# Optimization experiments

Measured on AMD Instinct MI355X. Metric: run time of the kernel, lower is better.

## Reference

```python
import jax, jax.numpy as jnp
import numpy as np

B, N, K = 4096, 64, 4


def _jump_sum(Ls, rho):
    # sum_k L_k @ rho @ L_k^dagger  (real dtype -> dagger == transpose)
    return jnp.einsum('kij,bjl,kml->bim', Ls, rho, Ls)


def _sandwich(U, rho):
    # U @ rho @ U^dagger
    return jnp.einsum('ij,bjl,ml->bim', U, rho, U)


def setup_inputs() -> dict:
    key = jax.random.key(0)
    k = jax.random.split(key, 6)
    eye = jnp.eye(N, dtype=jnp.float32)
    rho0 = jax.random.normal(k[0], (B, N, N), dtype=jnp.float32)
    # propagators: near-identity perturbations, Um well-conditioned for the LU solve
    U1 = eye + 0.1 * jax.random.normal(k[1], (N, N), dtype=jnp.float32)
    Um = eye + 0.1 * jax.random.normal(k[2], (N, N), dtype=jnp.float32)
    Ls0 = jax.random.normal(k[3], (K, N, N), dtype=jnp.float32)
    Lsmid = jax.random.normal(k[4], (K, N, N), dtype=jnp.float32)
    Ls1 = jax.random.normal(k[5], (K, N, N), dtype=jnp.float32)
    dt = jnp.asarray(0.01, dtype=jnp.float32)
    return {'rho0': rho0, 'U1': U1, 'Um': Um, 'Ls0': Ls0,
            'Lsmid': Lsmid, 'Ls1': Ls1, 'dt': dt}


def reference(rho0, U1, Um, Ls0, Lsmid, Ls1, dt):
    # propagator from t+dt/2 to t+dt via LU solve: solve(Um^T, U1^T)^T
    Um1 = jnp.linalg.solve(Um.T, U1.T).T

    # stage 1
    rho1 = rho0
    # stage 2 (SecondStage, no_jump_0 = Um, Ls = Ls0, aii = 0.5)
    rho2 = _sandwich(Um, rho0 + 0.5 * dt * _jump_sum(Ls0, rho1))
    # stage 3 (SameTimeStage, no_jump_0 = Um, Ls = Lsmid, aii = 0.5)
    rho3 = _sandwich(Um, rho0) + 0.5 * dt * _jump_sum(Lsmid, rho2)
    rho23 = rho2 + rho3
    # stage 4 (RKStage, no_jump_0 = U1, no_jump_i = Um1, Ls = Lsmid, aii = 1.0)
    rho4 = _sandwich(U1, rho0) + _sandwich(Um1, dt * _jump_sum(Lsmid, rho3))

    out = (_sandwich(U1, rho0 + (dt / 6) * _jump_sum(Ls0, rho1))
           + _sandwich(Um1, (dt / 3) * _jump_sum(Lsmid, rho23))
           + (dt / 6) * _jump_sum(Ls1, rho4))
    return out
```

## Files before the change

### kernel.cpp

```cpp
#include <hip/hip_runtime.h>


typedef __attribute__((ext_vector_type(16))) float f32x16;
typedef __attribute__((ext_vector_type(8))) __bf16 bf16x8;

#define MATB 8192

__device__ __forceinline__ unsigned short bf16rne(float x) {
  unsigned u = __builtin_bit_cast(unsigned, x);
  return (unsigned short)((u + 0x7FFFu + ((u >> 16) & 1u)) >> 16);
}
__device__ __forceinline__ float bflo(unsigned u) {
  return __builtin_bit_cast(float, u << 16);
}
__device__ __forceinline__ float bfhi(unsigned u) {
  return __builtin_bit_cast(float, u & 0xFFFF0000u);
}

__device__ __forceinline__ void mm4_gl(f32x16& acc, const char* __restrict__ gP,
                                       const char* ldsQ, int vq, int lh) {
#pragma unroll
  for (int s = 0; s < 4; ++s) {
    bf16x8 a = *(const bf16x8*)(gP + s * 1024);
    bf16x8 b = *(const bf16x8*)(ldsQ + (((2 * s + lh) ^ vq) << 4));
    acc = __builtin_amdgcn_mfma_f32_32x32x16_bf16(a, b, acc, 0, 0, 0);
  }
}
__device__ __forceinline__ void mm4_lg(f32x16& acc, const char* ldsP, int vp,
                                       int lh, const char* __restrict__ gQ) {
#pragma unroll
  for (int s = 0; s < 4; ++s) {
    bf16x8 a = *(const bf16x8*)(ldsP + (((2 * s + lh) ^ vp) << 4));
    bf16x8 b = *(const bf16x8*)(gQ + s * 1024);
    acc = __builtin_amdgcn_mfma_f32_32x32x16_bf16(a, b, acc, 0, 0, 0);
  }
}

__device__ __forceinline__ void wtile(char* base, int ti, int slotc, int coff,
                                      int lh, const f32x16& v) {
#pragma unroll
  for (int r = 0; r < 16; ++r) {
    int row = ti * 32 + 4 * lh + (r & 3) + 8 * (r >> 2);
    int ps = (slotc ^ ((4 * ti + (r >> 2)) & 7)) << 4;
    *(unsigned short*)(base + row * 128 + ps + coff) = bf16rne(v[r]);
  }
}
__device__ __forceinline__ void wtile_rmw(char* base, int ti, int slotc, int coff,
                                          int lh, const f32x16& v, float s) {
#pragma unroll
  for (int r = 0; r < 16; ++r) {
    int row = ti * 32 + 4 * lh + (r & 3) + 8 * (r >> 2);
    int ps = (slotc ^ ((4 * ti + (r >> 2)) & 7)) << 4;
    unsigned short* p = (unsigned short*)(base + row * 128 + ps + coff);
    float old = bflo((unsigned)*p);
    *p = bf16rne(old + s * v[r]);
  }
}

__device__ __forceinline__ void axpy(char* D, const char* A, float s,
                                     const char* B, int tid) {
#pragma unroll
  for (int j = 0; j < 8; ++j) {
    int off = (tid + 256 * j) * 4;
    unsigned a = *(const unsigned*)(A + off);
    unsigned b = *(const unsigned*)(B + off);
    float lo = bflo(a) + s * bflo(b);
    float hi = bfhi(a) + s * bfhi(b);
    *(unsigned*)(D + off) = (unsigned)bf16rne(lo) | ((unsigned)bf16rne(hi) << 16);
  }
}

__global__ __launch_bounds__(256) void kraus_invert(
    const float* __restrict__ U1, const float* __restrict__ Um,
    float* __restrict__ Um1) {
  __shared__ float M[64][66];
  __shared__ float X[64][66];
  int tid = threadIdx.x;
#pragma unroll
  for (int it = 0; it < 16; ++it) {
    int idx = tid + 256 * it;
    int r = idx >> 6, c = idx & 63;
    M[r][c] = Um[idx];
    X[r][c] = (r == c) ? 1.0f : 0.0f;
  }
  __syncthreads();
  for (int k = 0; k < 64; ++k) {
    if (tid < 64) {
      float ip = 1.0f / M[k][k];
      M[k][tid] *= ip;
      X[k][tid] *= ip;
    }
    __syncthreads();
    int r = tid & 63, q = tid >> 6;
    float f = M[r][k];
    __syncthreads();
    if (r != k) {
#pragma unroll
      for (int cc = 0; cc < 16; ++cc) {
        int c = q * 16 + cc;
        M[r][c] -= f * M[k][c];
        X[r][c] -= f * X[k][c];
      }
    }
    __syncthreads();
  }
  for (int it = 0; it < 16; ++it) {
    int idx = tid + 256 * it;
    int i = idx >> 6, j = idx & 63;
    float s = 0.0f;
#pragma unroll 4
    for (int k = 0; k < 64; ++k) s += U1[i * 64 + k] * X[k][j];
    Um1[idx] = s;
  }
}

__global__ __launch_bounds__(256) void kraus_prepack(
    const float* __restrict__ U1, const float* __restrict__ Um,
    const float* __restrict__ Ls0, const float* __restrict__ Lsmid,
    const float* __restrict__ Ls1, float* __restrict__ ws) {
  const float* Um1 = ws;
  unsigned short* dst = (unsigned short*)((char*)ws + 16384);
  int o = blockIdx.x;
  const float* s;
  if (o == 0) s = U1;
  else if (o == 1) s = Um;
  else if (o == 2) s = Um1;
  else if (o < 7) s = Ls0 + (o - 3) * 4096;
  else if (o < 11) s = Lsmid + (o - 7) * 4096;
  else s = Ls1 + (o - 11) * 4096;
  unsigned short* d = dst + o * 4096;
  int tid = threadIdx.x;
#pragma unroll
  for (int j = 0; j < 16; ++j) {
    int idx = tid + 256 * j;
    int f = idx >> 9, l = (idx >> 3) & 63, i = idx & 7;
    int t = f >> 2, ss = f & 3;
    int R = t * 32 + (l & 31);
    int C = ss * 16 + (l >> 5) * 8 + i;
    d[idx] = bf16rne(s[R * 64 + C]);
  }
}

__global__ __launch_bounds__(256, 4) void kraus_main(
    const float* __restrict__ rho0g, const float* __restrict__ dtp,
    const char* __restrict__ gfrag, float* __restrict__ outg) {
  __shared__ __align__(16) char lds[5 * MATB];
  char* B0 = lds;
  char* B1 = B0 + MATB;
  char* B3 = B1 + MATB;
  char* B4 = B3 + MATB;
  char* TMP = B4 + MATB;

  const int tid = threadIdx.x;
  const int l = tid & 63, w = tid >> 6;
  const int ti = w >> 1, tj = w & 1;
  const int l31 = l & 31, lh = l >> 5;
  const int vA = (4 * ti + (l31 >> 3)) & 7;
  const int vB = (4 * tj + (l31 >> 3)) & 7;
  const int rA = (ti * 32 + l31) * 128;
  const int rB = (tj * 32 + l31) * 128;
  const int slotc = 4 * tj + (l31 >> 3), coff = (l31 & 7) * 2;
  const float dt = dtp[0];
  const size_t b = blockIdx.x;
  const char* gA0 = gfrag + ti * 4096 + l * 16;
  const char* gB0 = gfrag + tj * 4096 + l * 16;
#define GA(o) (gA0 + (o) * 8192)
#define GB(o) (gB0 + (o) * 8192)

  {
    const float* src = rho0g + b * 4096 + tid * 16;
    float vals[16];
#pragma unroll
    for (int q = 0; q < 4; ++q) {
      float4 f = *(const float4*)(src + q * 4);
      vals[q * 4 + 0] = f.x; vals[q * 4 + 1] = f.y;
      vals[q * 4 + 2] = f.z; vals[q * 4 + 3] = f.w;
    }
    int r = tid >> 2, c0 = (tid & 3) * 16;
    int sr = r >> 3, cr = (r & 7) * 2;
#pragma unroll
    for (int u = 0; u < 16; ++u) {
      int row = c0 + u;
      int ps = (sr ^ ((row >> 3) & 7)) << 4;
      *(unsigned short*)(B0 + row * 128 + ps + cr) = bf16rne(vals[u]);
    }
  }
  __syncthreads();

  f32x16 outacc = {};

  {
    f32x16 J = {};
    for (int k = 0; k < 4; ++k) {
      if (k) __syncthreads();
      f32x16 t = {};
      mm4_gl(t, GA(3 + k), B0 + rB, vB, lh);
      wtile(TMP, ti, slotc, coff, lh, t);
      __syncthreads();
      mm4_gl(J, GA(3 + k), TMP + rB, vB, lh);
    }
    __syncthreads();
    wtile(B1, ti, slotc, coff, lh, J);
  }
  __syncthreads();

  { f32x16 t = {}; mm4_gl(t, GA(0), B1 + rB, vB, lh); wtile(TMP, ti, slotc, coff, lh, t); }
  __syncthreads();
  { f32x16 s = {}; mm4_lg(s, TMP + rA, vA, lh, GB(0)); outacc += (dt / 6.f) * s; }
  __syncthreads();

  { f32x16 t = {}; mm4_gl(t, GA(0), B0 + rB, vB, lh); wtile(TMP, ti, slotc, coff, lh, t); }
  __syncthreads();
  { f32x16 s = {}; mm4_lg(s, TMP + rA, vA, lh, GB(0)); outacc += s; }
  { f32x16 s = {}; mm4_gl(s, GA(0), TMP + rB, vB, lh); wtile(B4, ti, slotc, coff, lh, s); }

  axpy(B1, B0, 0.5f * dt, B1, tid);
  __syncthreads();

  { f32x16 t = {}; mm4_gl(t, GA(1), B1 + rB, vB, lh); wtile(TMP, ti, slotc, coff, lh, t); }
  __syncthreads();
  { f32x16 s = {}; mm4_gl(s, GA(1), TMP + rB, vB, lh); wtile(B1, ti, slotc, coff, lh, s); }
  __syncthreads();

  { f32x16 t = {}; mm4_gl(t, GA(1), B0 + rB, vB, lh); wtile(TMP, ti, slotc, coff, lh, t); }
  __syncthreads();
  { f32x16 s = {}; mm4_gl(s, GA(1), TMP + rB, vB, lh); wtile(B3, ti, slotc, coff, lh, s); }
  __syncthreads();

  {
    f32x16 J = {};
    for (int k = 0; k < 4; ++k) {
      if (k) __syncthreads();
      f32x16 t = {};
      mm4_gl(t, GA(7 + k), B1 + rB, vB, lh);
      wtile(TMP, ti, slotc, coff, lh, t);
      __syncthreads();
      mm4_gl(J, GA(7 + k), TMP + rB, vB, lh);
    }
    __syncthreads();
    wtile(B0, ti, slotc, coff, lh, J);
  }
  __syncthreads();
  axpy(B1, B3, 0.5f * dt, B0, tid);
  __syncthreads();

  {
    f32x16 J = {};
    for (int k = 0; k < 4; ++k) {
      if (k) __syncthreads();
      f32x16 t = {};
      mm4_gl(t, GA(7 + k), B1 + rB, vB, lh);
      wtile(TMP, ti, slotc, coff, lh, t);
      __syncthreads();
      mm4_gl(J, GA(7 + k), TMP + rB, vB, lh);
    }
    __syncthreads();
    wtile(B3, ti, slotc, coff, lh, J);
  }
  __syncthreads();
  axpy(B1, B0, 1.0f, B3, tid);
  __syncthreads();

  { f32x16 t = {}; mm4_gl(t, GA(2), B1 + rB, vB, lh); wtile(TMP, ti, slotc, coff, lh, t); }
  __syncthreads();
  { f32x16 s = {}; mm4_lg(s, TMP + rA, vA, lh, GB(2)); outacc += (dt / 3.f) * s; }
  __syncthreads();

  { f32x16 t = {}; mm4_gl(t, GA(2), B3 + rB, vB, lh); wtile(TMP, ti, slotc, coff, lh, t); }
  __syncthreads();
  { f32x16 s = {}; mm4_gl(s, GA(2), TMP + rB, vB, lh); wtile_rmw(B4, ti, slotc, coff, lh, s, dt); }
  __syncthreads();

  {
    f32x16 J = {};
    for (int k = 0; k < 4; ++k) {
      if (k) __syncthreads();
      f32x16 t = {};
      mm4_gl(t, GA(11 + k), B4 + rB, vB, lh);
      wtile(TMP, ti, slotc, coff, lh, t);
      __syncthreads();
      mm4_lg(J, TMP + rA, vA, lh, GB(11 + k));
    }
    outacc += (dt / 6.f) * J;
  }

  {
    float* op = outg + b * 4096 + (size_t)(ti * 32 + lh * 4) * 64 + tj * 32 + l31;
#pragma unroll
    for (int r = 0; r < 16; ++r) {
      int row = (r & 3) + 8 * (r >> 2);
      op[row * 64] = outacc[r];
    }
  }
#undef GA
#undef GB
}

extern "C" void kernel_launch(void* const* d_in, const int* in_sizes, int n_in,
                              void* d_out, int out_size, void* d_ws, size_t ws_size,
                              hipStream_t stream) {
  const float* rho0 = (const float*)d_in[0];
  const float* U1 = (const float*)d_in[1];
  const float* Um = (const float*)d_in[2];
  const float* Ls0 = (const float*)d_in[3];
  const float* Lsmid = (const float*)d_in[4];
  const float* Ls1 = (const float*)d_in[5];
  const float* dtp = (const float*)d_in[6];
  float* out = (float*)d_out;
  float* ws = (float*)d_ws;

  const int B = in_sizes[0] >> 12;

  kraus_invert<<<1, 256, 0, stream>>>(U1, Um, ws);
  kraus_prepack<<<15, 256, 0, stream>>>(U1, Um, Ls0, Lsmid, Ls1, ws);
  kraus_main<<<B, 256, 0, stream>>>(rho0, dtp, (const char*)d_ws + 16384, out);
}
```

Before: 232.6 us.

## Double-buffer jump-sum intermediates and merge independent stages to cut barriers

```diff
diff --git a/kernel.cpp b/kernel.cpp
--- a/kernel.cpp
+++ b/kernel.cpp
@@ -164,8 +164,14 @@
   const size_t b = blockIdx.x;
   const char* gA0 = gfrag + ti * 4096 + l * 16;
   const char* gB0 = gfrag + tj * 4096 + l * 16;
-#define GA(o) (gA0 + (o) * 8192)
-#define GB(o) (gB0 + (o) * 8192)
+
+  auto GL = [&](f32x16& acc, int op, const char* q) {
+    mm4_gl(acc, gA0 + op * 8192, q + rB, vB, lh);
+  };
+  auto LG = [&](f32x16& acc, const char* p, int op) {
+    mm4_lg(acc, p + rA, vA, lh, gB0 + op * 8192);
+  };
+  auto WT = [&](char* dst, const f32x16& v) { wtile(dst, ti, slotc, coff, lh, v); };
 
   {
     const float* src = rho0g + b * 4096 + tid * 16;
@@ -191,97 +197,68 @@
 
   {
     f32x16 J = {};
-    for (int k = 0; k < 4; ++k) {
-      if (k) __syncthreads();
-      f32x16 t = {};
-      mm4_gl(t, GA(3 + k), B0 + rB, vB, lh);
-      wtile(TMP, ti, slotc, coff, lh, t);
-      __syncthreads();
-      mm4_gl(J, GA(3 + k), TMP + rB, vB, lh);
-    }
-    __syncthreads();
-    wtile(B1, ti, slotc, coff, lh, J);
-  }
-  __syncthreads();
-
-  { f32x16 t = {}; mm4_gl(t, GA(0), B1 + rB, vB, lh); wtile(TMP, ti, slotc, coff, lh, t); }
-  __syncthreads();
-  { f32x16 s = {}; mm4_lg(s, TMP + rA, vA, lh, GB(0)); outacc += (dt / 6.f) * s; }
-  __syncthreads();
-
-  { f32x16 t = {}; mm4_gl(t, GA(0), B0 + rB, vB, lh); wtile(TMP, ti, slotc, coff, lh, t); }
-  __syncthreads();
-  { f32x16 s = {}; mm4_lg(s, TMP + rA, vA, lh, GB(0)); outacc += s; }
-  { f32x16 s = {}; mm4_gl(s, GA(0), TMP + rB, vB, lh); wtile(B4, ti, slotc, coff, lh, s); }
-
-  axpy(B1, B0, 0.5f * dt, B1, tid);
-  __syncthreads();
-
-  { f32x16 t = {}; mm4_gl(t, GA(1), B1 + rB, vB, lh); wtile(TMP, ti, slotc, coff, lh, t); }
-  __syncthreads();
-  { f32x16 s = {}; mm4_gl(s, GA(1), TMP + rB, vB, lh); wtile(B1, ti, slotc, coff, lh, s); }
-  __syncthreads();
-
-  { f32x16 t = {}; mm4_gl(t, GA(1), B0 + rB, vB, lh); wtile(TMP, ti, slotc, coff, lh, t); }
-  __syncthreads();
-  { f32x16 s = {}; mm4_gl(s, GA(1), TMP + rB, vB, lh); wtile(B3, ti, slotc, coff, lh, s); }
-  __syncthreads();
-
-  {
-    f32x16 J = {};
-    for (int k = 0; k < 4; ++k) {
-      if (k) __syncthreads();
-      f32x16 t = {};
-      mm4_gl(t, GA(7 + k), B1 + rB, vB, lh);
-      wtile(TMP, ti, slotc, coff, lh, t);
-      __syncthreads();
-      mm4_gl(J, GA(7 + k), TMP + rB, vB, lh);
-    }
-    __syncthreads();
-    wtile(B0, ti, slotc, coff, lh, J);
-  }
-  __syncthreads();
-  axpy(B1, B3, 0.5f * dt, B0, tid);
-  __syncthreads();
-
-  {
-    f32x16 J = {};
-    for (int k = 0; k < 4; ++k) {
-      if (k) __syncthreads();
-      f32x16 t = {};
-      mm4_gl(t, GA(7 + k), B1 + rB, vB, lh);
-      wtile(TMP, ti, slotc, coff, lh, t);
-      __syncthreads();
-      mm4_gl(J, GA(7 + k), TMP + rB, vB, lh);
-    }
-    __syncthreads();
-    wtile(B3, ti, slotc, coff, lh, J);
-  }
-  __syncthreads();
-  axpy(B1, B0, 1.0f, B3, tid);
-  __syncthreads();
-
-  { f32x16 t = {}; mm4_gl(t, GA(2), B1 + rB, vB, lh); wtile(TMP, ti, slotc, coff, lh, t); }
-  __syncthreads();
-  { f32x16 s = {}; mm4_lg(s, TMP + rA, vA, lh, GB(2)); outacc += (dt / 3.f) * s; }
-  __syncthreads();
-
-  { f32x16 t = {}; mm4_gl(t, GA(2), B3 + rB, vB, lh); wtile(TMP, ti, slotc, coff, lh, t); }
-  __syncthreads();
-  { f32x16 s = {}; mm4_gl(s, GA(2), TMP + rB, vB, lh); wtile_rmw(B4, ti, slotc, coff, lh, s, dt); }
-  __syncthreads();
-
-  {
-    f32x16 J = {};
-    for (int k = 0; k < 4; ++k) {
-      if (k) __syncthreads();
-      f32x16 t = {};
-      mm4_gl(t, GA(11 + k), B4 + rB, vB, lh);
-      wtile(TMP, ti, slotc, coff, lh, t);
-      __syncthreads();
-      mm4_lg(J, TMP + rA, vA, lh, GB(11 + k));
-    }
-    outacc += (dt / 6.f) * J;
+    { f32x16 t = {}; GL(t, 3, B0); WT(TMP, t); } __syncthreads();
+    { f32x16 t = {}; GL(J, 3, TMP); GL(t, 4, B0); WT(B1, t); } __syncthreads();
+    { f32x16 t = {}; GL(J, 4, B1); GL(t, 5, B0); WT(TMP, t); } __syncthreads();
+    { f32x16 t = {}; GL(J, 5, TMP); GL(t, 6, B0); WT(B1, t); } __syncthreads();
+    { GL(J, 6, B1); WT(TMP, J); } __syncthreads();
+  }
+
+  { f32x16 t = {}; GL(t, 0, TMP); WT(B1, t); axpy(B4, B0, 0.5f * dt, TMP, tid); }
+  __syncthreads();
+
+  { f32x16 s = {}; LG(s, B1, 0); outacc += (dt / 6.f) * s;
+    f32x16 t = {}; GL(t, 0, B0); WT(TMP, t); }
+  __syncthreads();
+
+  { f32x16 s = {}; LG(s, TMP, 0); outacc += s;
+    f32x16 p = {}; GL(p, 0, TMP); WT(B1, p);
+    f32x16 t = {}; GL(t, 1, B4); WT(B3, t); }
+  __syncthreads();
+
+  { f32x16 r2 = {}; GL(r2, 1, B3); WT(B4, r2);
+    f32x16 t = {}; GL(t, 1, B0); WT(TMP, t); }
+  __syncthreads();
+
+  { f32x16 s = {}; GL(s, 1, TMP); WT(B0, s);
+    f32x16 t = {}; GL(t, 7, B4); WT(B3, t); }
+  __syncthreads();
+
+  {
+    f32x16 J = {};
+    { f32x16 t = {}; GL(J, 7, B3); GL(t, 8, B4); WT(TMP, t); } __syncthreads();
+    { f32x16 t = {}; GL(J, 8, TMP); GL(t, 9, B4); WT(B3, t); } __syncthreads();
+    { f32x16 t = {}; GL(J, 9, B3); GL(t, 10, B4); WT(TMP, t); } __syncthreads();
+    { GL(J, 10, TMP); WT(B4, J); } __syncthreads();
+  }
+
+  axpy(B0, B0, 0.5f * dt, B4, tid);
+  __syncthreads();
+
+  {
+    f32x16 J = {};
+    { f32x16 t = {}; GL(t, 7, B0); WT(TMP, t); } __syncthreads();
+    { f32x16 t = {}; GL(J, 7, TMP); GL(t, 8, B0); WT(B3, t); } __syncthreads();
+    { f32x16 t = {}; GL(J, 8, B3); GL(t, 9, B0); WT(TMP, t); } __syncthreads();
+    { f32x16 t = {}; GL(J, 9, TMP); GL(t, 10, B0); WT(B3, t); } __syncthreads();
+    { GL(J, 10, B3); WT(TMP, J); } __syncthreads();
+  }
+
+  { f32x16 a = {}; GL(a, 2, TMP); f32x16 c = a; GL(c, 2, B4);
+    WT(B0, a); WT(B3, c); }
+  __syncthreads();
+
+  { f32x16 s = {}; LG(s, B3, 2); outacc += (dt / 3.f) * s;
+    f32x16 q = {}; GL(q, 2, B0); wtile_rmw(B1, ti, slotc, coff, lh, q, dt); }
+  __syncthreads();
+
+  {
+    f32x16 J = {};
+    { f32x16 t = {}; GL(t, 11, B1); WT(TMP, t); } __syncthreads();
+    { f32x16 t = {}; LG(J, TMP, 11); GL(t, 12, B1); WT(B4, t); } __syncthreads();
+    { f32x16 t = {}; LG(J, B4, 12); GL(t, 13, B1); WT(TMP, t); } __syncthreads();
+    { f32x16 t = {}; LG(J, TMP, 13); GL(t, 14, B1); WT(B4, t); } __syncthreads();
+    { LG(J, B4, 14); outacc += (dt / 6.f) * J; }
   }
 
   {
@@ -292,8 +269,6 @@
       op[row * 64] = outacc[r];
     }
   }
-#undef GA
-#undef GB
 }
 
 extern "C" void kernel_launch(void* const* d_in, const int* in_sizes, int n_in,
```

Result: no change. 233.8 us (+0.5%).
